# Performance work log

Measured on AMD Instinct MI355X. Metric: run time of the kernel, lower is better.

## Reference

```python
import jax, jax.numpy as jnp
import numpy as np

B, S, D = 4, 4096, 2048
H, HD = 16, 128
TILE = 16
N_TILES = 8


def setup_inputs() -> dict:
    key = jax.random.key(0)
    ks = jax.random.split(key, 6)
    x = jax.random.normal(ks[0], (B, S, D), dtype=jnp.float32)
    anchor_indices = jax.random.randint(ks[1], (B, H, N_TILES), 0, S // TILE).astype(jnp.int32)
    sc = 1.0 / np.sqrt(D)
    Wq = jax.random.normal(ks[2], (D, H * HD), dtype=jnp.float32) * sc
    Wk = jax.random.normal(ks[3], (D, H * HD), dtype=jnp.float32) * sc
    Wv = jax.random.normal(ks[4], (D, H * HD), dtype=jnp.float32) * sc
    Wo = jax.random.normal(ks[5], (H * HD, D), dtype=jnp.float32) * (1.0 / np.sqrt(H * HD))
    return {"x": x, "anchor_indices": anchor_indices, "Wq": Wq, "Wk": Wk, "Wv": Wv, "Wo": Wo}


def reference(x, anchor_indices, Wq, Wk, Wv, Wo):
    batch, seq_len, _ = x.shape
    # QKV projections -> (b, h, s, d)
    q = (x @ Wq).reshape(batch, seq_len, H, HD).transpose(0, 2, 1, 3)
    k = (x @ Wk).reshape(batch, seq_len, H, HD).transpose(0, 2, 1, 3)
    v = (x @ Wv).reshape(batch, seq_len, H, HD).transpose(0, 2, 1, 3)
    # Force last tile slot to the current local tile (causal local attention)
    current_tile_idx = (seq_len - 1) // TILE
    tiles = anchor_indices.at[:, :, -1].set(current_tile_idx)
    # Expand tile indices to token indices: (b, h, n_tiles*TILE)
    token_indices = (tiles[..., None] * TILE + jnp.arange(TILE)[None, None, None, :]).reshape(batch, H, -1)
    # Gather sparse K/V per head: (b, h, K, d)
    k_sparse = jnp.take_along_axis(k, token_indices[..., None], axis=2)
    v_sparse = jnp.take_along_axis(v, token_indices[..., None], axis=2)
    logits = jnp.einsum('bhqd,bhkd->bhqk', q, k_sparse) / jnp.sqrt(jnp.float32(HD))
    # Causal mask over gathered (non-contiguous) key positions
    future_mask = token_indices[:, :, None, :] > jnp.arange(seq_len)[None, None, :, None]
    logits = jnp.where(future_mask, -1e10, logits)
    weights = jax.nn.softmax(logits, axis=-1)
    out = jnp.einsum('bhqk,bhkd->bhqd', weights, v_sparse)
    out = out.transpose(0, 2, 1, 3).reshape(batch, seq_len, H * HD)
    return out @ Wo
```

## Files before the change

kernel.cpp:

```cpp
#include <hip/hip_runtime.h>
#include <stdint.h>

#define Bz 4
#define Sz 4096
#define Dz 2048
#define Hz 16
#define HDz 128
#define NTz 8
#define TILEz 16

typedef __bf16 bf16x8 __attribute__((ext_vector_type(8)));
typedef float f32x4 __attribute__((ext_vector_type(4)));
typedef float fx4 __attribute__((ext_vector_type(4)));
typedef unsigned short u16;
typedef u16 u16x4 __attribute__((ext_vector_type(4)));
typedef u16 u16x8 __attribute__((ext_vector_type(8)));

#define MFMA16(a, b, c) __builtin_amdgcn_mfma_f32_16x16x32_bf16((a), (b), (c), 0, 0, 0)

__device__ __forceinline__ u16 f2bf(float f) {
    uint32_t u = __builtin_bit_cast(uint32_t, f);
    return (u16)((u + 0x7fffu + ((u >> 16) & 1u)) >> 16);
}

__device__ __forceinline__ void async16(const u16* g, u16* l) {
    __builtin_amdgcn_global_load_lds(
        (const __attribute__((address_space(1))) unsigned int*)(g),
        (__attribute__((address_space(3))) unsigned int*)(l), 16, 0, 0);
}

#define BAR()                                  \
    do {                                       \
        asm volatile("" ::: "memory");         \
        __builtin_amdgcn_s_barrier();          \
        asm volatile("" ::: "memory");         \
    } while (0)

__global__ void cvt_x(const float* __restrict__ x, u16* __restrict__ o) {
    int i = blockIdx.x * 256 + threadIdx.x;
    const fx4* xv = (const fx4*)x;
    fx4 a = xv[i * 2], b = xv[i * 2 + 1];
    u16x8 r;
    r[0] = f2bf(a[0]); r[1] = f2bf(a[1]); r[2] = f2bf(a[2]); r[3] = f2bf(a[3]);
    r[4] = f2bf(b[0]); r[5] = f2bf(b[1]); r[6] = f2bf(b[2]); r[7] = f2bf(b[3]);
    ((u16x8*)o)[i] = r;
}

__global__ void transpose_cvt(const float* W0, const float* W1, const float* W2, const float* W3,
                              u16* O0, u16* O1, u16* O2, u16* O3) {
    const float* W; u16* O;
    switch (blockIdx.z) {
        case 0: W = W0; O = O0; break;
        case 1: W = W1; O = O1; break;
        case 2: W = W2; O = O2; break;
        default: W = W3; O = O3; break;
    }
    __shared__ u16 tile[32][33];
    int bx = blockIdx.x * 32, by = blockIdx.y * 32;
    int tx = threadIdx.x, ty = threadIdx.y;
#pragma unroll
    for (int i = 0; i < 32; i += 8)
        tile[ty + i][tx] = f2bf(W[(long)(by + ty + i) * 2048 + bx + tx]);
    __syncthreads();
#pragma unroll
    for (int i = 0; i < 32; i += 8)
        O[(long)(bx + ty + i) * 2048 + by + tx] = tile[tx][ty + i];
}

__device__ __forceinline__ void stage2(const u16* s0, const u16* s1, u16* chunk, int w, int koff) {
    async16(s0 + koff, chunk + w * 512);
    async16(s1 + koff, chunk + w * 512 + 4096);
}

template <typename OutT>
__global__ __launch_bounds__(512, 2) void gemm256(const u16* __restrict__ A, const u16* __restrict__ BT,
                                                  OutT* __restrict__ C, int M_, int N_, int K_) {
    __shared__ __align__(1024) u16 lds[65536];
    const int t = threadIdx.x, w = t >> 6, l = t & 63, lr = l & 15, quad = l >> 4;
    const int wm = w >> 2, wn = w & 3;
    const int nbn = N_ >> 8;
    const int cpx = gridDim.x >> 3;
    const int swz = (blockIdx.x & 7) * cpx + (blockIdx.x >> 3);
    const int bm = swz / nbn, bn = swz % nbn;

    const u16* sA[2]; const u16* sB[2];
#pragma unroll
    for (int r = 0; r < 2; r++) {
        int idx = r * 512 + t;
        int row = idx >> 2;
        int q = (t & 3) ^ ((row >> 2) & 2);
        sA[r] = A + (long)(bm * 256 + row) * K_ + q * 8;
        sB[r] = BT + (long)(bn * 256 + row) * K_ + q * 8;
    }
    const int qro = (quad ^ (((lr >> 3) & 1) << 1)) * 8;
    const int rowA0 = wm * 128 + lr;
    const int rowB0 = wn * 64 + lr;
    const int nt = K_ >> 6;

    f32x4 acc[8][4] = {};

    stage2(sA[0], sA[1], lds + 0, w, 0);
    stage2(sB[0], sB[1], lds + 32768, w, 0);
    stage2(sA[0], sA[1], lds + 8192, w, 32);
    stage2(sB[0], sB[1], lds + 32768 + 8192, w, 32);
    const int k1 = (nt > 1) ? 64 : 0;
    stage2(sA[0], sA[1], lds + 16384, w, k1);
    stage2(sB[0], sB[1], lds + 32768 + 16384, w, k1);
    asm volatile("s_waitcnt vmcnt(4)" ::: "memory");
    BAR();

    for (int g = 0; g < nt; ++g) {
        const int cb = g & 1, ob = cb ^ 1;
        const int t1k = ((g + 1 < nt ? g + 1 : nt - 1) << 6) + 32;
        const int t2k = ((g + 2 < nt ? g + 2 : nt - 1) << 6);
        const u16* Abase = lds + cb * 16384;
        const u16* Bbase = lds + 32768 + cb * 16384;
#pragma unroll
        for (int kh = 0; kh < 2; ++kh) {
            const u16* Ach = Abase + kh * 8192;
            const u16* Bch = Bbase + kh * 8192;
            bf16x8 bfr[4];
#pragma unroll
            for (int j = 0; j < 4; ++j)
                bfr[j] = *(const bf16x8*)(Bch + (rowB0 + j * 16) * 32 + qro);
#pragma unroll
            for (int mh = 0; mh < 2; ++mh) {
                bf16x8 af[4];
#pragma unroll
                for (int i = 0; i < 4; ++i)
                    af[i] = *(const bf16x8*)(Ach + (rowA0 + mh * 64 + i * 16) * 32 + qro);
                if (kh == 0 && mh == 0)      stage2(sA[0], sA[1], lds + ob * 16384 + 8192, w, t1k);
                else if (kh == 0 && mh == 1) stage2(sB[0], sB[1], lds + 32768 + ob * 16384 + 8192, w, t1k);
                else if (kh == 1 && mh == 0) stage2(sA[0], sA[1], lds + cb * 16384, w, t2k);
                else                         stage2(sB[0], sB[1], lds + 32768 + cb * 16384, w, t2k);
                asm volatile("" ::: "memory");
                __builtin_amdgcn_s_barrier();
                asm volatile("s_waitcnt lgkmcnt(0)" ::: "memory");
                __builtin_amdgcn_s_setprio(1);
#pragma unroll
                for (int i = 0; i < 4; ++i)
#pragma unroll
                    for (int j = 0; j < 4; ++j)
                        acc[mh * 4 + i][j] = MFMA16(af[i], bfr[j], acc[mh * 4 + i][j]);
                __builtin_amdgcn_s_setprio(0);
                if (kh == 1 && mh == 1) asm volatile("s_waitcnt vmcnt(4)" ::: "memory");
                BAR();
            }
        }
    }

    const long crow0 = (long)bm * 256 + wm * 128;
    const int ccol0 = bn * 256 + wn * 64;
#pragma unroll
    for (int f = 0; f < 8; ++f) {
        long row0 = crow0 + (f >> 2) * 64 + (f & 3) * 16 + quad * 4;
#pragma unroll
        for (int j = 0; j < 4; ++j) {
            int col = ccol0 + j * 16 + lr;
#pragma unroll
            for (int rg = 0; rg < 4; ++rg) {
                long idx = (row0 + rg) * N_ + col;
                if constexpr (sizeof(OutT) == 2) ((u16*)C)[idx] = f2bf(acc[f][j][rg]);
                else ((float*)C)[idx] = acc[f][j][rg];
            }
        }
    }
}

#define KV_SPLIT 4
#define KV_CHUNK (Dz / KV_SPLIT)
__global__ __launch_bounds__(256) void kv_sparse(const u16* __restrict__ xbf, const u16* __restrict__ WkT,
                                                 const u16* __restrict__ WvT, const int* __restrict__ anchor,
                                                 float* __restrict__ part) {
    const int bh = blockIdx.x, which = blockIdx.y, split = blockIdx.z;
    const int b = bh >> 4, h = bh & 15;
    __shared__ int toks[128];
    __shared__ __align__(16) u16 As[4096];
    __shared__ __align__(16) u16 Bs[4096];
    const int t = threadIdx.x, w = t >> 6, l = t & 63, lr = l & 15, quad = l >> 4;
    if (t < 128) {
        int j = t >> 4;
        int tile = (j == 7) ? (Sz / TILEz - 1) : anchor[bh * NTz + j];
        toks[t] = tile * TILEz + (t & 15);
    }
    __syncthreads();
    const u16* gA[2]; const u16* gB[2]; u16* lA[2]; u16* lB[2];
#pragma unroll
    for (int r = 0; r < 2; r++) {
        int c = r * 256 + t;
        int row = c >> 2, col8 = (c & 3) * 8;
        const u16* xrow = xbf + ((long)b * Sz + toks[row]) * Dz + col8;
        const u16* wrowK = WkT + (long)(h * HDz + row) * Dz + col8;
        const u16* wrowV = WvT + (long)(h * HDz + row) * Dz + col8;
        gA[r] = (which == 0) ? xrow : wrowV;
        gB[r] = (which == 0) ? wrowK : xrow;
        lA[r] = &As[(r * 256 + w * 64) * 8];
        lB[r] = &Bs[(r * 256 + w * 64) * 8];
    }
    f32x4 acc[4][4] = {};
    const int wr = (w >> 1) * 64, wc = (w & 1) * 64;
    const int ks0 = split * KV_CHUNK;
    for (int k0 = ks0; k0 < ks0 + KV_CHUNK; k0 += 32) {
        async16(gA[0] + k0, lA[0]); async16(gA[1] + k0, lA[1]);
        async16(gB[0] + k0, lB[0]); async16(gB[1] + k0, lB[1]);
        __syncthreads();
        bf16x8 af[4], bfr[4];
#pragma unroll
        for (int i = 0; i < 4; i++) af[i] = *(const bf16x8*)&As[(wr + i * 16 + lr) * 32 + quad * 8];
#pragma unroll
        for (int j = 0; j < 4; j++) bfr[j] = *(const bf16x8*)&Bs[(wc + j * 16 + lr) * 32 + quad * 8];
#pragma unroll
        for (int i = 0; i < 4; i++)
#pragma unroll
            for (int j = 0; j < 4; j++) acc[i][j] = MFMA16(af[i], bfr[j], acc[i][j]);
        __syncthreads();
    }
    float* out = part + (((long)split * 2 + which) * 64 + bh) * 16384;
#pragma unroll
    for (int i = 0; i < 4; i++) {
        int row0 = wr + i * 16 + quad * 4;
#pragma unroll
        for (int j = 0; j < 4; j++) {
            int col = wc + j * 16 + lr;
#pragma unroll
            for (int rg = 0; rg < 4; rg++) out[(row0 + rg) * 128 + col] = acc[i][j][rg];
        }
    }
}

__global__ void kv_reduce(const float* __restrict__ part, u16* __restrict__ kv) {
    long i = ((long)blockIdx.x * 256 + threadIdx.x) * 4;
    const long stride = 2L * 64 * 16384;
    fx4 s = *(const fx4*)(part + i);
#pragma unroll
    for (int sp = 1; sp < KV_SPLIT; sp++) {
        fx4 p = *(const fx4*)(part + sp * stride + i);
        s[0] += p[0]; s[1] += p[1]; s[2] += p[2]; s[3] += p[3];
    }
    u16x4 r;
    r[0] = f2bf(s[0]); r[1] = f2bf(s[1]); r[2] = f2bf(s[2]); r[3] = f2bf(s[3]);
    *(u16x4*)(kv + i) = r;
}

__global__ __launch_bounds__(256) void attn_kernel(u16* QAO,
                                                   const u16* __restrict__ ksp, const u16* __restrict__ vspT,
                                                   const int* __restrict__ anchor) {
    const int st = blockIdx.x, h = blockIdx.y, b = blockIdx.z;
    const int bh = b * Hz + h, s0 = st * 128;
    __shared__ __align__(16) u16 Ps[128 * 136];
    __shared__ int toks[128];
    const int t = threadIdx.x, w = t >> 6, l = t & 63, lr = l & 15, quad = l >> 4;
    if (t < 128) {
        int j = t >> 4;
        int tile = (j == 7) ? (Sz / TILEz - 1) : anchor[bh * NTz + j];
        toks[t] = tile * TILEz + (t & 15);
    }
    __syncthreads();
    const u16* Qb = QAO + (long)(b * Sz + s0 + w * 32) * 2048 + h * HDz;
    const u16* Kb = ksp + (long)bh * HDz * 128;
    const u16* Vb = vspT + (long)bh * HDz * 128;
    f32x4 acc[2][8] = {};
#pragma unroll
    for (int ks = 0; ks < 4; ks++) {
        bf16x8 a0 = *(const bf16x8*)(Qb + (long)lr * 2048 + ks * 32 + quad * 8);
        bf16x8 a1 = *(const bf16x8*)(Qb + (long)(16 + lr) * 2048 + ks * 32 + quad * 8);
#pragma unroll
        for (int j = 0; j < 8; j++) {
            bf16x8 bj = *(const bf16x8*)(Kb + (j * 16 + lr) * 128 + ks * 32 + quad * 8);
            acc[0][j] = MFMA16(a0, bj, acc[0][j]);
            acc[1][j] = MFMA16(a1, bj, acc[1][j]);
        }
    }
    int tokj[8];
#pragma unroll
    for (int j = 0; j < 8; j++) tokj[j] = toks[j * 16 + lr];
    const float scale = 0.08838834764831845f;
#pragma unroll
    for (int i = 0; i < 2; i++) {
#pragma unroll
        for (int rg = 0; rg < 4; rg++) {
            int qpos = s0 + w * 32 + i * 16 + quad * 4 + rg;
            float v[8];
#pragma unroll
            for (int j = 0; j < 8; j++)
                v[j] = (tokj[j] > qpos) ? -1e10f : acc[i][j][rg] * scale;
            float mx = v[0];
#pragma unroll
            for (int j = 1; j < 8; j++) mx = fmaxf(mx, v[j]);
            mx = fmaxf(mx, __shfl_xor(mx, 1, 64));
            mx = fmaxf(mx, __shfl_xor(mx, 2, 64));
            mx = fmaxf(mx, __shfl_xor(mx, 4, 64));
            mx = fmaxf(mx, __shfl_xor(mx, 8, 64));
            float s = 0.f;
#pragma unroll
            for (int j = 0; j < 8; j++) { v[j] = exp2f((v[j] - mx) * 1.4426950408889634f); s += v[j]; }
            s += __shfl_xor(s, 1, 64);
            s += __shfl_xor(s, 2, 64);
            s += __shfl_xor(s, 4, 64);
            s += __shfl_xor(s, 8, 64);
            float rs = 1.0f / s;
            int prow = w * 32 + i * 16 + quad * 4 + rg;
#pragma unroll
            for (int j = 0; j < 8; j++) Ps[prow * 136 + j * 16 + lr] = f2bf(v[j] * rs);
        }
    }
    __syncthreads();
    f32x4 oacc[2][8] = {};
#pragma unroll
    for (int ks = 0; ks < 4; ks++) {
        bf16x8 a0 = *(const bf16x8*)(Vb + (w * 32 + lr) * 128 + ks * 32 + quad * 8);
        bf16x8 a1 = *(const bf16x8*)(Vb + (w * 32 + 16 + lr) * 128 + ks * 32 + quad * 8);
#pragma unroll
        for (int j = 0; j < 8; j++) {
            bf16x8 bj = *(const bf16x8*)&Ps[(j * 16 + lr) * 136 + ks * 32 + quad * 8];
            oacc[0][j] = MFMA16(a0, bj, oacc[0][j]);
            oacc[1][j] = MFMA16(a1, bj, oacc[1][j]);
        }
    }
#pragma unroll
    for (int i = 0; i < 2; i++) {
#pragma unroll
        for (int j = 0; j < 8; j++) {
            u16x4 pk;
#pragma unroll
            for (int rg = 0; rg < 4; rg++) pk[rg] = f2bf(oacc[i][j][rg]);
            int d = w * 32 + i * 16 + quad * 4;
            int q = j * 16 + lr;
            *(u16x4*)(QAO + (long)(b * Sz + s0 + q) * 2048 + h * HDz + d) = pk;
        }
    }
}

extern "C" void kernel_launch(void* const* d_in, const int* in_sizes, int n_in,
                              void* d_out, int out_size, void* d_ws, size_t ws_size,
                              hipStream_t stream) {
    const float* x = (const float*)d_in[0];
    const int* anchor = (const int*)d_in[1];
    const float* Wq = (const float*)d_in[2];
    const float* Wk = (const float*)d_in[3];
    const float* Wv = (const float*)d_in[4];
    const float* Wo = (const float*)d_in[5];

    char* ws = (char*)d_ws;
    const size_t XB = 67108864;
    const size_t WB = 8388608;
    u16* xbf = (u16*)(ws);
    u16* WqT = (u16*)(ws + XB);
    u16* WkT = (u16*)(ws + XB + WB);
    u16* WvT = (u16*)(ws + XB + 2 * WB);
    u16* WoT = (u16*)(ws + XB + 3 * WB);
    u16* Qb  = (u16*)(ws + XB + 4 * WB);
    float* kvpart = (float*)(ws + XB + 4 * WB);
    u16* ksp = (u16*)(ws + 2 * XB + 4 * WB);
    u16* vspT= (u16*)(ws + 2 * XB + 4 * WB + 2097152);

    cvt_x<<<16384, 256, 0, stream>>>(x, xbf);
    transpose_cvt<<<dim3(64, 64, 4), dim3(32, 8), 0, stream>>>(Wq, Wk, Wv, Wo, WqT, WkT, WvT, WoT);
    kv_sparse<<<dim3(64, 2, KV_SPLIT), 256, 0, stream>>>(xbf, WkT, WvT, anchor, kvpart);
    kv_reduce<<<2048, 256, 0, stream>>>(kvpart, ksp);
    gemm256<u16><<<dim3(512), dim3(512), 0, stream>>>(xbf, WqT, Qb, 16384, 2048, 2048);
    attn_kernel<<<dim3(32, 16, 4), 256, 0, stream>>>(Qb, ksp, vspT, anchor);
    gemm256<float><<<dim3(512), dim3(512), 0, stream>>>(Qb, WoT, (float*)d_out, 16384, 2048, 2048);
}
```

Before: 628.8 us.

## Stage sparse K in swizzled LDS and use 512-thread attention blocks

The attention kernel now uses 8 waves per block, each owning 16 query rows instead of 4 waves owning 32. The 32 KB per-head sparse K block is copied once into LDS with async loads and an XOR swizzle, so each wave no longer re-reads K from global memory. Q and V fragments are preloaded into registers, and the V loads are issued before the barrier so they overlap with it. This cuts redundant global K traffic and register accumulators per thread, but raises LDS use per block, which may lower block occupancy.

```diff
diff --git a/kernel.cpp b/kernel.cpp
--- a/kernel.cpp
+++ b/kernel.cpp
@@ -242,11 +242,12 @@
     *(u16x4*)(kv + i) = r;
 }
 
-__global__ __launch_bounds__(256) void attn_kernel(u16* QAO,
+__global__ __launch_bounds__(512) void attn_kernel(u16* QAO,
                                                    const u16* __restrict__ ksp, const u16* __restrict__ vspT,
                                                    const int* __restrict__ anchor) {
     const int st = blockIdx.x, h = blockIdx.y, b = blockIdx.z;
     const int bh = b * Hz + h, s0 = st * 128;
+    __shared__ __align__(16) u16 Kl[16384];
     __shared__ __align__(16) u16 Ps[128 * 136];
     __shared__ int toks[128];
     const int t = threadIdx.x, w = t >> 6, l = t & 63, lr = l & 15, quad = l >> 4;
@@ -255,20 +256,28 @@
         int tile = (j == 7) ? (Sz / TILEz - 1) : anchor[bh * NTz + j];
         toks[t] = tile * TILEz + (t & 15);
     }
-    __syncthreads();
-    const u16* Qb = QAO + (long)(b * Sz + s0 + w * 32) * 2048 + h * HDz;
+    const u16* Qb = QAO + (long)(b * Sz + s0 + w * 16) * 2048 + h * HDz;
     const u16* Kb = ksp + (long)bh * HDz * 128;
     const u16* Vb = vspT + (long)bh * HDz * 128;
-    f32x4 acc[2][8] = {};
+    bf16x8 qf[4];
+#pragma unroll
+    for (int ks = 0; ks < 4; ks++)
+        qf[ks] = *(const bf16x8*)(Qb + (long)lr * 2048 + ks * 32 + quad * 8);
+#pragma unroll
+    for (int r = 0; r < 4; r++) {
+        int idx = r * 512 + t;
+        int row = idx >> 4, c = idx & 15;
+        async16(Kb + row * 128 + ((c ^ (row & 7)) * 8), Kl + (r * 512 + w * 64) * 8);
+    }
+    __syncthreads();
+    f32x4 acc[8] = {};
 #pragma unroll
     for (int ks = 0; ks < 4; ks++) {
-        bf16x8 a0 = *(const bf16x8*)(Qb + (long)lr * 2048 + ks * 32 + quad * 8);
-        bf16x8 a1 = *(const bf16x8*)(Qb + (long)(16 + lr) * 2048 + ks * 32 + quad * 8);
 #pragma unroll
         for (int j = 0; j < 8; j++) {
-            bf16x8 bj = *(const bf16x8*)(Kb + (j * 16 + lr) * 128 + ks * 32 + quad * 8);
-            acc[0][j] = MFMA16(a0, bj, acc[0][j]);
-            acc[1][j] = MFMA16(a1, bj, acc[1][j]);
+            int kr = j * 16 + lr;
+            bf16x8 bj = *(const bf16x8*)(Kl + kr * 128 + (((ks * 4 + quad) ^ (lr & 7)) * 8));
+            acc[j] = MFMA16(qf[ks], bj, acc[j]);
         }
     }
     int tokj[8];
@@ -276,58 +285,53 @@
     for (int j = 0; j < 8; j++) tokj[j] = toks[j * 16 + lr];
     const float scale = 0.08838834764831845f;
 #pragma unroll
-    for (int i = 0; i < 2; i++) {
-#pragma unroll
-        for (int rg = 0; rg < 4; rg++) {
-            int qpos = s0 + w * 32 + i * 16 + quad * 4 + rg;
-            float v[8];
-#pragma unroll
-            for (int j = 0; j < 8; j++)
-                v[j] = (tokj[j] > qpos) ? -1e10f : acc[i][j][rg] * scale;
-            float mx = v[0];
-#pragma unroll
-            for (int j = 1; j < 8; j++) mx = fmaxf(mx, v[j]);
-            mx = fmaxf(mx, __shfl_xor(mx, 1, 64));
-            mx = fmaxf(mx, __shfl_xor(mx, 2, 64));
-            mx = fmaxf(mx, __shfl_xor(mx, 4, 64));
-            mx = fmaxf(mx, __shfl_xor(mx, 8, 64));
-            float s = 0.f;
-#pragma unroll
-            for (int j = 0; j < 8; j++) { v[j] = exp2f((v[j] - mx) * 1.4426950408889634f); s += v[j]; }
-            s += __shfl_xor(s, 1, 64);
-            s += __shfl_xor(s, 2, 64);
-            s += __shfl_xor(s, 4, 64);
-            s += __shfl_xor(s, 8, 64);
-            float rs = 1.0f / s;
-            int prow = w * 32 + i * 16 + quad * 4 + rg;
-#pragma unroll
-            for (int j = 0; j < 8; j++) Ps[prow * 136 + j * 16 + lr] = f2bf(v[j] * rs);
-        }
-    }
+    for (int rg = 0; rg < 4; rg++) {
+        int qpos = s0 + w * 16 + quad * 4 + rg;
+        float v[8];
+#pragma unroll
+        for (int j = 0; j < 8; j++)
+            v[j] = (tokj[j] > qpos) ? -1e10f : acc[j][rg] * scale;
+        float mx = v[0];
+#pragma unroll
+        for (int j = 1; j < 8; j++) mx = fmaxf(mx, v[j]);
+        mx = fmaxf(mx, __shfl_xor(mx, 1, 64));
+        mx = fmaxf(mx, __shfl_xor(mx, 2, 64));
+        mx = fmaxf(mx, __shfl_xor(mx, 4, 64));
+        mx = fmaxf(mx, __shfl_xor(mx, 8, 64));
+        float s = 0.f;
+#pragma unroll
+        for (int j = 0; j < 8; j++) { v[j] = exp2f((v[j] - mx) * 1.4426950408889634f); s += v[j]; }
+        s += __shfl_xor(s, 1, 64);
+        s += __shfl_xor(s, 2, 64);
+        s += __shfl_xor(s, 4, 64);
+        s += __shfl_xor(s, 8, 64);
+        float rs = 1.0f / s;
+        int prow = w * 16 + quad * 4 + rg;
+#pragma unroll
+        for (int j = 0; j < 8; j++) Ps[prow * 136 + j * 16 + lr] = f2bf(v[j] * rs);
+    }
+    bf16x8 va[4];
+#pragma unroll
+    for (int ks = 0; ks < 4; ks++)
+        va[ks] = *(const bf16x8*)(Vb + (w * 16 + lr) * 128 + ks * 32 + quad * 8);
     __syncthreads();
-    f32x4 oacc[2][8] = {};
+    f32x4 oacc[8] = {};
 #pragma unroll
     for (int ks = 0; ks < 4; ks++) {
-        bf16x8 a0 = *(const bf16x8*)(Vb + (w * 32 + lr) * 128 + ks * 32 + quad * 8);
-        bf16x8 a1 = *(const bf16x8*)(Vb + (w * 32 + 16 + lr) * 128 + ks * 32 + quad * 8);
 #pragma unroll
         for (int j = 0; j < 8; j++) {
-            bf16x8 bj = *(const bf16x8*)&Ps[(j * 16 + lr) * 136 + ks * 32 + quad * 8];
-            oacc[0][j] = MFMA16(a0, bj, oacc[0][j]);
-            oacc[1][j] = MFMA16(a1, bj, oacc[1][j]);
-        }
-    }
-#pragma unroll
-    for (int i = 0; i < 2; i++) {
-#pragma unroll
-        for (int j = 0; j < 8; j++) {
-            u16x4 pk;
-#pragma unroll
-            for (int rg = 0; rg < 4; rg++) pk[rg] = f2bf(oacc[i][j][rg]);
-            int d = w * 32 + i * 16 + quad * 4;
-            int q = j * 16 + lr;
-            *(u16x4*)(QAO + (long)(b * Sz + s0 + q) * 2048 + h * HDz + d) = pk;
-        }
+            bf16x8 pj = *(const bf16x8*)&Ps[(j * 16 + lr) * 136 + ks * 32 + quad * 8];
+            oacc[j] = MFMA16(va[ks], pj, oacc[j]);
+        }
+    }
+#pragma unroll
+    for (int j = 0; j < 8; j++) {
+        u16x4 pk;
+#pragma unroll
+        for (int rg = 0; rg < 4; rg++) pk[rg] = f2bf(oacc[j][rg]);
+        int d = w * 16 + quad * 4;
+        int q = j * 16 + lr;
+        *(u16x4*)(QAO + (long)(b * Sz + s0 + q) * 2048 + h * HDz + d) = pk;
     }
 }
 
@@ -359,6 +363,6 @@
     kv_sparse<<<dim3(64, 2, KV_SPLIT), 256, 0, stream>>>(xbf, WkT, WvT, anchor, kvpart);
     kv_reduce<<<2048, 256, 0, stream>>>(kvpart, ksp);
     gemm256<u16><<<dim3(512), dim3(512), 0, stream>>>(xbf, WqT, Qb, 16384, 2048, 2048);
-    attn_kernel<<<dim3(32, 16, 4), 256, 0, stream>>>(Qb, ksp, vspT, anchor);
+    attn_kernel<<<dim3(32, 16, 4), dim3(512), 0, stream>>>(Qb, ksp, vspT, anchor);
     gemm256<float><<<dim3(512), dim3(512), 0, stream>>>(Qb, WoT, (float*)d_out, 16384, 2048, 2048);
 }
```

Measured after the change: 600.8 us. -4.5%, faster.
